# Optimization experiments

Hardware: AMD Instinct MI355X
Metric: run time of the kernel (lower is better)

## Reference

```python
import jax, jax.numpy as jnp
import numpy as np
from jax import lax

BIG = jnp.float32(1e8)  # stand-in for +inf (no zeros found yet)
EPS_W = 1e-3
SMOOTH = 1e-6
ALPHA = 0.6
BETA = 1.0


def _scan_dist(zmask):
    # zmask: (H, B, W) bool, True where pixel == 0.
    # Forward 1D chamfer pass along leading axis: exact 1D distance to nearest zero.
    def body(c, z):
        d = jnp.where(z, jnp.float32(0.0), c + jnp.float32(1.0))
        return d, d
    init = jnp.full(zmask.shape[1:], BIG, jnp.float32)
    _, out = lax.scan(body, init, zmask)
    return out  # (H, B, W)


def edt(t):
    # Exact Euclidean distance transform (distance to nearest zero), t: (B, H, W).
    # Separable Felzenszwalb-style: exact 1D pass along H, then lower-envelope
    # (brute-force min via scan) along W on squared distances.
    z = (t == 0)
    zm = jnp.moveaxis(z, 1, 0)                      # (H, B, W)
    fwd = _scan_dist(zm)
    bwd = _scan_dist(zm[::-1])[::-1]
    d1 = jnp.minimum(fwd, bwd)                      # 1D distance along H
    g = jnp.minimum(d1 * d1, BIG)                   # squared, (H, B, W)

    W = g.shape[-1]
    ys = jnp.arange(W, dtype=jnp.float32)
    g_cols = jnp.moveaxis(g, 2, 0)                  # (W, H, B)

    def body2(carry, xs):
        gcol, j = xs                                # gcol: (H, B)
        cand = gcol[..., None] + (ys - j) ** 2      # (H, B, W)
        return jnp.minimum(carry, cand), None

    init = jnp.full(g.shape, BIG, jnp.float32)
    out, _ = lax.scan(body2, init, (g_cols, ys))    # (H, B, W) squared EDT
    return jnp.sqrt(jnp.moveaxis(out, 1, 0))        # (B, H, W)


def setup_inputs() -> dict:
    key = jax.random.key(0)
    k1, k2 = jax.random.split(key)
    B, C, H, W = 16, 1, 512, 512
    inputs = jax.random.normal(k1, (B, C, H, W), dtype=jnp.float32)
    targets = jax.random.randint(k2, (B, C, H, W), 0, 2).astype(jnp.float32)
    return {"inputs": inputs, "targets": targets}


def reference(inputs, targets):
    B = targets.shape[0]
    t2d = targets[:, 0]                             # (B, H, W), squeeze channel
    w_edt = edt(t2d)                                # per-sample EDT, (B, H, W)
    v = jnp.max(w_edt, axis=(1, 2))                 # scalar max per sample
    # Faithful to original (buggy) indexing: w = v - w_edt[b] (row b, shape (W,))
    rows = w_edt[jnp.arange(B), jnp.arange(B), :]   # (B, W)
    mask = (w_edt != 0).astype(jnp.float32)         # (B, H, W)
    w = mask * (v[:, None, None] - rows[:, None, :]) + jnp.float32(EPS_W)
    weight = lax.stop_gradient(w)[:, None, :, :]    # (B, 1, H, W); no grad (numpy in orig)

    wmse = jnp.mean(weight * (inputs - targets) ** 2)

    p = jax.nn.sigmoid(inputs).reshape(-1)
    tg = targets.reshape(-1)
    intersection = jnp.sum(p * tg)
    union = jnp.sum(p) + jnp.sum(tg)
    dice = 1.0 - (2.0 * intersection + SMOOTH) / (union + SMOOTH)

    return (ALPHA * wmse, BETA * dice)
```

## Files before the change

kernel.cpp:

```cpp
#include <hip/hip_runtime.h>

#define W      512
#define IMG    (512 * 512)
#define NB     16
#define NPIX   (NB * IMG)

#define TILE_H 16
#define APRON  4
#define LROWS  (TILE_H + 2 * APRON)
#define BLOCK  1024
#define GRID   (NB * (W / TILE_H))

struct WS {
    unsigned int vmax[16];
    float C[NB * W];
    float rows[NB * W];
    float4 partial[GRID];
};
#define MEMSET_BYTES (sizeof(unsigned int) * 16 + sizeof(float) * NB * W)

__device__ __forceinline__ unsigned pk_min_u16(unsigned a, unsigned b) {
    unsigned r; asm("v_pk_min_u16 %0, %1, %2" : "=v"(r) : "v"(a), "v"(b)); return r;
}
__device__ __forceinline__ unsigned pk_max_u16(unsigned a, unsigned b) {
    unsigned r; asm("v_pk_max_u16 %0, %1, %2" : "=v"(r) : "v"(a), "v"(b)); return r;
}

__device__ int exact_best(const float* __restrict__ img, int h, int y) {
    int best = 100000000;
    for (int gh = 0; gh < W; ++gh) {
        int dhh = gh - h;
        if (dhh * dhh >= best) continue;
        const float* rp = img + (gh << 9);
        for (int yy = 0; yy < W; ++yy)
            if (rp[yy] == 0.0f) {
                int dx = yy - y;
                best = min(best, dhh * dhh + dx * dx);
            }
    }
    return best;
}

__global__ __launch_bounds__(BLOCK, 8) void fused_kernel(const float* __restrict__ inp,
                                                         const float* __restrict__ tgt,
                                                         WS* __restrict__ ws) {
    __shared__ unsigned long long zm[LROWS][10];
    __shared__ unsigned short Dd[LROWS][W];
    __shared__ float4 csh[8][128];
    __shared__ float4 ssum[BLOCK / 64];
    __shared__ unsigned smax[BLOCK / 64];

    int bid  = blockIdx.x;
    int b    = bid >> 5;
    int tile = bid & 31;
    int h0   = tile * TILE_H;
    int tid  = threadIdx.x;
    int wave = tid >> 6, lane = tid & 63;
    const float* img = tgt + (size_t)b * IMG;

    float av[4];
    #pragma unroll
    for (int j = 0; j < 4; ++j) {
        int aa = (wave << 2) + j;
        int ar = aa >> 3;
        int lr = ar < 4 ? ar : ar + 16;
        int wc = aa & 7;
        int gh = h0 - APRON + lr;
        av[j] = (gh >= 0 && gh < W) ? img[(gh << 9) + (wc << 6) + lane] : 1.0f;
    }

    size_t base4 = (size_t)b * (IMG / 4) + (size_t)tile * (TILE_H * W / 4);
    const float4* x4 = (const float4*)inp + base4;
    const float4* t4 = (const float4*)tgt + base4;

    float s0 = 0.f, s1 = 0.f, s2 = 0.f, s3 = 0.f;
    float4 ct = make_float4(0.f, 0.f, 0.f, 0.f);
    #pragma unroll
    for (int k = 0; k < 2; ++k) {
        int i = tid + (k << 10);
        float4 xv = x4[i];
        float4 tv = t4[i];
        { float d = xv.x - tv.x; float e2 = d * d; s0 += e2; ct.x += tv.x * e2;
          float p = 1.0f / (1.0f + __expf(-xv.x)); s1 += p * tv.x; s2 += p; s3 += tv.x; }
        { float d = xv.y - tv.y; float e2 = d * d; s0 += e2; ct.y += tv.y * e2;
          float p = 1.0f / (1.0f + __expf(-xv.y)); s1 += p * tv.y; s2 += p; s3 += tv.y; }
        { float d = xv.z - tv.z; float e2 = d * d; s0 += e2; ct.z += tv.z * e2;
          float p = 1.0f / (1.0f + __expf(-xv.z)); s1 += p * tv.z; s2 += p; s3 += tv.z; }
        { float d = xv.w - tv.w; float e2 = d * d; s0 += e2; ct.w += tv.w * e2;
          float p = 1.0f / (1.0f + __expf(-xv.w)); s1 += p * tv.w; s2 += p; s3 += tv.w; }

        unsigned nib = (tv.x == 0.f ? 1u : 0u) | (tv.y == 0.f ? 2u : 0u)
                     | (tv.z == 0.f ? 4u : 0u) | (tv.w == 0.f ? 8u : 0u);
        unsigned long long contrib = (unsigned long long)nib << ((lane & 15) << 2);
        #pragma unroll
        for (int m = 1; m <= 8; m <<= 1) contrib |= __shfl_xor(contrib, m);
        if ((lane & 15) == 0) {
            int r = (wave >> 1) + (k << 3);
            zm[APRON + r][((wave & 1) << 2) + (lane >> 4) + 1] = contrib;
        }
    }
    csh[tid >> 7][tid & 127] = ct;
    #pragma unroll
    for (int o = 32; o > 0; o >>= 1) {
        s0 += __shfl_down(s0, o); s1 += __shfl_down(s1, o);
        s2 += __shfl_down(s2, o); s3 += __shfl_down(s3, o);
    }
    if (lane == 0) ssum[wave] = make_float4(s0, s1, s2, s3);

    #pragma unroll
    for (int j = 0; j < 4; ++j) {
        int aa = (wave << 2) + j;
        int ar = aa >> 3;
        int lr = ar < 4 ? ar : ar + 16;
        int wc = aa & 7;
        unsigned long long m = __ballot(av[j] == 0.0f);
        if (lane == 0) zm[lr][wc + 1] = m;
    }
    if (tid < LROWS) { zm[tid][0] = 0ULL; zm[tid][9] = 0ULL; }
    __syncthreads();

    for (int u = wave; u < LROWS * 8; u += BLOCK / 64) {
        int lr = u >> 3, wc = u & 7;
        unsigned long long Wm = zm[lr][wc];
        unsigned long long Wc = zm[lr][wc + 1];
        unsigned long long Wp = zm[lr][wc + 2];
        int off = lane;
        unsigned long long wr = (Wc >> off) | (off ? (Wp << (64 - off)) : 0ULL);
        int dr = wr ? __builtin_ctzll(wr) : 1000;
        unsigned long long vl = off ? ((Wc << (64 - off)) | (Wm >> off)) : Wm;
        int dl = vl ? (1 + __builtin_clzll(vl)) : 1000;
        int d = min(min(dr, dl), 1000);
        int dd = min(d * d, 65471);
        Dd[lr][(wc << 6) + lane] = (unsigned short)dd;
    }

    if (tid < 128) {
        float4 a = csh[0][tid];
        #pragma unroll
        for (int g = 1; g < 8; ++g) {
            float4 c = csh[g][tid];
            a.x += c.x; a.y += c.y; a.z += c.z; a.w += c.w;
        }
        float* Cb = ws->C + (b << 9) + (tid << 2);
        atomicAdd(Cb + 0, a.x);
        atomicAdd(Cb + 1, a.y);
        atomicAdd(Cb + 2, a.z);
        atomicAdd(Cb + 3, a.w);
    } else if (tid == 128) {
        float4 a = ssum[0];
        #pragma unroll
        for (int i = 1; i < BLOCK / 64; ++i) {
            a.x += ssum[i].x; a.y += ssum[i].y; a.z += ssum[i].z; a.w += ssum[i].w;
        }
        ws->partial[bid] = a;
    }
    __syncthreads();

    int p = tid & 255;
    int q = tid >> 8;
    const unsigned* Dd32 = (const unsigned*)&Dd[0][0];
    const unsigned* basep = Dd32 + (q << 10) + p;
    unsigned col[12];
    #pragma unroll
    for (int j = 0; j < 12; ++j) col[j] = basep[j * 256];

    unsigned best[4];
    #pragma unroll
    for (int m = 0; m < 4; ++m) {
        unsigned bb = 0xFFFFFFFFu;
        #pragma unroll
        for (int j = 0; j <= 8; ++j) {
            unsigned dh2 = (unsigned)((j - 4) * (j - 4));
            bb = pk_min_u16(bb, col[m + j] + dh2 * 0x00010001u);
        }
        best[m] = bb;
    }
    unsigned bpk = pk_max_u16(pk_max_u16(best[0], best[1]), pk_max_u16(best[2], best[3]));
    unsigned tmax = max(bpk & 0xFFFFu, bpk >> 16);

    if (__builtin_expect(tmax > 16u, 0)) {
        tmax = 0;
        for (int m = 0; m < 4; ++m) {
            int k = (q << 2) + m;
            unsigned nb = 0;
            for (int half = 0; half < 2; ++half) {
                int y = (p << 1) + half;
                int bb = 1 << 30;
                for (int j = 0; j <= 8; ++j)
                    bb = min(bb, (j - 4) * (j - 4) + (int)Dd[k + j][y]);
                if (bb > 16) bb = exact_best(img, h0 + k, y);
                tmax = max(tmax, (unsigned)bb);
                nb |= ((unsigned)bb & 0xFFFFu) << (half * 16);
            }
            best[m] = nb;
        }
    }

    if (tile == 0 && q == (b >> 2)) {
        unsigned rb = best[b & 3];
        ws->rows[(b << 9) + (p << 1)]     = sqrtf((float)(rb & 0xFFFFu));
        ws->rows[(b << 9) + (p << 1) + 1] = sqrtf((float)(rb >> 16));
    }

    #pragma unroll
    for (int o = 32; o > 0; o >>= 1) tmax = max(tmax, (unsigned)__shfl_down(tmax, o));
    if (lane == 0) smax[wave] = tmax;
    __syncthreads();
    if (tid == 0) {
        unsigned bm = smax[0];
        #pragma unroll
        for (int i = 1; i < BLOCK / 64; ++i) bm = max(bm, smax[i]);
        atomicMax(&ws->vmax[b], bm);
    }
}

#define FBLOCK 256
__global__ __launch_bounds__(FBLOCK) void final_kernel(const WS* __restrict__ ws,
                                                       float* __restrict__ out) {
    int tid = threadIdx.x;
    __shared__ float vsh[16];
    if (tid < 16) vsh[tid] = sqrtf((float)ws->vmax[tid]);
    __syncthreads();

    double wm = 0.0;
    #pragma unroll
    for (int j = 0; j < (NB * W) / FBLOCK; ++j) {
        int cell = tid + j * FBLOCK;
        wm += (double)ws->C[cell] * (double)(vsh[cell >> 9] - ws->rows[cell]);
    }
    double e = 0, s1 = 0, s2 = 0, s3 = 0;
    #pragma unroll
    for (int j = 0; j < GRID / FBLOCK; ++j) {
        float4 p = ws->partial[tid + j * FBLOCK];
        e += p.x; s1 += p.y; s2 += p.z; s3 += p.w;
    }

    #pragma unroll
    for (int o = 32; o > 0; o >>= 1) {
        wm += __shfl_down(wm, o); e  += __shfl_down(e, o);
        s1 += __shfl_down(s1, o); s2 += __shfl_down(s2, o); s3 += __shfl_down(s3, o);
    }
    __shared__ double shd[FBLOCK / 64][5];
    int lane = tid & 63, wid = tid >> 6;
    if (lane == 0) { shd[wid][0] = wm; shd[wid][1] = e;
                     shd[wid][2] = s1; shd[wid][3] = s2; shd[wid][4] = s3; }
    __syncthreads();
    if (tid == 0) {
        double a0 = 0, a1 = 0, a2 = 0, a3 = 0, a4 = 0;
        #pragma unroll
        for (int i = 0; i < FBLOCK / 64; ++i) {
            a0 += shd[i][0]; a1 += shd[i][1]; a2 += shd[i][2]; a3 += shd[i][3]; a4 += shd[i][4];
        }
        double wmse = (a0 + 0.001 * a1) / (double)NPIX;
        out[0] = (float)(0.6 * wmse);
        out[1] = (float)(1.0 - (2.0 * a2 + 1e-6) / (a3 + a4 + 1e-6));
    }
}

extern "C" void kernel_launch(void* const* d_in, const int* in_sizes, int n_in,
                              void* d_out, int out_size, void* d_ws, size_t ws_size,
                              hipStream_t stream) {
    const float* inp = (const float*)d_in[0];
    const float* tgt = (const float*)d_in[1];
    float* out = (float*)d_out;
    WS* ws = (WS*)d_ws;

    hipMemsetAsync(d_ws, 0, MEMSET_BYTES, stream);
    fused_kernel<<<GRID, BLOCK, 0, stream>>>(inp, tgt, ws);
    final_kernel<<<1, FBLOCK, 0, stream>>>(ws, out);
}
```

Baseline: 90.10 us.

## Replace atomics and memset with per-block partials and multi-block final reduction

Each fused block now writes its column partial sums, per-wave scalar sums and per-wave maxima to dedicated workspace slots instead of using float atomicAdd/atomicMax. This removes the hipMemsetAsync launch and the in-block reduction syncs. The final kernel runs one block per image to reduce those partials, and the last block, found through a wrap-around atomic counter, combines the 16 per-image results. This trades atomic contention and a memset for more workspace traffic and a counter that is never reset, which relies on the modulo-16 check staying valid across calls.

New measurement: 90.76 us. No clear change (+0.7%).

```diff
diff --git a/kernel.cpp b/kernel.cpp
--- a/kernel.cpp
+++ b/kernel.cpp
@@ -12,12 +12,13 @@
 #define GRID   (NB * (W / TILE_H))
 
 struct WS {
-    unsigned int vmax[16];
-    float C[NB * W];
     float rows[NB * W];
-    float4 partial[GRID];
+    float4 colpart[GRID][128];
+    float4 partial[GRID][16];
+    unsigned wsmax[GRID][16];
+    double img5[NB][5];
+    unsigned counter;
 };
-#define MEMSET_BYTES (sizeof(unsigned int) * 16 + sizeof(float) * NB * W)
 
 __device__ __forceinline__ unsigned pk_min_u16(unsigned a, unsigned b) {
     unsigned r; asm("v_pk_min_u16 %0, %1, %2" : "=v"(r) : "v"(a), "v"(b)); return r;
@@ -47,8 +48,6 @@
     __shared__ unsigned long long zm[LROWS][10];
     __shared__ unsigned short Dd[LROWS][W];
     __shared__ float4 csh[8][128];
-    __shared__ float4 ssum[BLOCK / 64];
-    __shared__ unsigned smax[BLOCK / 64];
 
     int bid  = blockIdx.x;
     int b    = bid >> 5;
@@ -105,7 +104,7 @@
         s0 += __shfl_down(s0, o); s1 += __shfl_down(s1, o);
         s2 += __shfl_down(s2, o); s3 += __shfl_down(s3, o);
     }
-    if (lane == 0) ssum[wave] = make_float4(s0, s1, s2, s3);
+    if (lane == 0) ws->partial[bid][wave] = make_float4(s0, s1, s2, s3);
 
     #pragma unroll
     for (int j = 0; j < 4; ++j) {
@@ -141,18 +140,7 @@
             float4 c = csh[g][tid];
             a.x += c.x; a.y += c.y; a.z += c.z; a.w += c.w;
         }
-        float* Cb = ws->C + (b << 9) + (tid << 2);
-        atomicAdd(Cb + 0, a.x);
-        atomicAdd(Cb + 1, a.y);
-        atomicAdd(Cb + 2, a.z);
-        atomicAdd(Cb + 3, a.w);
-    } else if (tid == 128) {
-        float4 a = ssum[0];
-        #pragma unroll
-        for (int i = 1; i < BLOCK / 64; ++i) {
-            a.x += ssum[i].x; a.y += ssum[i].y; a.z += ssum[i].z; a.w += ssum[i].w;
-        }
-        ws->partial[bid] = a;
+        ws->colpart[bid][tid] = a;
     }
     __syncthreads();
 
@@ -204,52 +192,83 @@
 
     #pragma unroll
     for (int o = 32; o > 0; o >>= 1) tmax = max(tmax, (unsigned)__shfl_down(tmax, o));
-    if (lane == 0) smax[wave] = tmax;
-    __syncthreads();
-    if (tid == 0) {
-        unsigned bm = smax[0];
-        #pragma unroll
-        for (int i = 1; i < BLOCK / 64; ++i) bm = max(bm, smax[i]);
-        atomicMax(&ws->vmax[b], bm);
-    }
+    if (lane == 0) ws->wsmax[bid][wave] = tmax;
 }
 
 #define FBLOCK 256
-__global__ __launch_bounds__(FBLOCK) void final_kernel(const WS* __restrict__ ws,
+__global__ __launch_bounds__(FBLOCK) void final_kernel(WS* __restrict__ ws,
                                                        float* __restrict__ out) {
-    int tid = threadIdx.x;
-    __shared__ float vsh[16];
-    if (tid < 16) vsh[tid] = sqrtf((float)ws->vmax[tid]);
-    __syncthreads();
-
-    double wm = 0.0;
-    #pragma unroll
-    for (int j = 0; j < (NB * W) / FBLOCK; ++j) {
-        int cell = tid + j * FBLOCK;
-        wm += (double)ws->C[cell] * (double)(vsh[cell >> 9] - ws->rows[cell]);
-    }
-    double e = 0, s1 = 0, s2 = 0, s3 = 0;
-    #pragma unroll
-    for (int j = 0; j < GRID / FBLOCK; ++j) {
-        float4 p = ws->partial[tid + j * FBLOCK];
-        e += p.x; s1 += p.y; s2 += p.z; s3 += p.w;
-    }
+    int b    = blockIdx.x;
+    int tid  = threadIdx.x;
+    int lane = tid & 63, wave = tid >> 6;
+    __shared__ unsigned vsh4[4];
+    __shared__ double shd[4][5];
+    __shared__ double fin[80];
+    __shared__ int sh_last;
+
+    unsigned vm = 0;
+    #pragma unroll
+    for (int j = 0; j < 2; ++j) {
+        int idx = (tid << 1) + j;
+        vm = max(vm, ws->wsmax[(b << 5) + (idx >> 4)][idx & 15]);
+    }
+    #pragma unroll
+    for (int o = 32; o > 0; o >>= 1) vm = max(vm, (unsigned)__shfl_down(vm, o));
+    if (lane == 0) vsh4[wave] = vm;
+    __syncthreads();
+    float v = sqrtf((float)max(max(vsh4[0], vsh4[1]), max(vsh4[2], vsh4[3])));
+
+    double e = 0, t1 = 0, t2 = 0, t3 = 0;
+    #pragma unroll
+    for (int j = 0; j < 2; ++j) {
+        int idx = (tid << 1) + j;
+        float4 pp = ws->partial[(b << 5) + (idx >> 4)][idx & 15];
+        e += pp.x; t1 += pp.y; t2 += pp.z; t3 += pp.w;
+    }
+
+    int y4 = tid & 127, half = tid >> 7;
+    float4 acc = make_float4(0.f, 0.f, 0.f, 0.f);
+    #pragma unroll
+    for (int t = 0; t < 16; ++t) {
+        float4 cp = ws->colpart[(b << 5) + (half << 4) + t][y4];
+        acc.x += cp.x; acc.y += cp.y; acc.z += cp.z; acc.w += cp.w;
+    }
+    const float4 r4 = *(const float4*)&ws->rows[(b << 9) + (y4 << 2)];
+    double wm = (double)acc.x * (double)(v - r4.x) + (double)acc.y * (double)(v - r4.y)
+              + (double)acc.z * (double)(v - r4.z) + (double)acc.w * (double)(v - r4.w);
 
     #pragma unroll
     for (int o = 32; o > 0; o >>= 1) {
         wm += __shfl_down(wm, o); e  += __shfl_down(e, o);
-        s1 += __shfl_down(s1, o); s2 += __shfl_down(s2, o); s3 += __shfl_down(s3, o);
-    }
-    __shared__ double shd[FBLOCK / 64][5];
-    int lane = tid & 63, wid = tid >> 6;
-    if (lane == 0) { shd[wid][0] = wm; shd[wid][1] = e;
-                     shd[wid][2] = s1; shd[wid][3] = s2; shd[wid][4] = s3; }
+        t1 += __shfl_down(t1, o); t2 += __shfl_down(t2, o); t3 += __shfl_down(t3, o);
+    }
+    if (lane == 0) { shd[wave][0] = wm; shd[wave][1] = e;
+                     shd[wave][2] = t1; shd[wave][3] = t2; shd[wave][4] = t3; }
     __syncthreads();
     if (tid == 0) {
         double a0 = 0, a1 = 0, a2 = 0, a3 = 0, a4 = 0;
         #pragma unroll
-        for (int i = 0; i < FBLOCK / 64; ++i) {
+        for (int i = 0; i < 4; ++i) {
             a0 += shd[i][0]; a1 += shd[i][1]; a2 += shd[i][2]; a3 += shd[i][3]; a4 += shd[i][4];
+        }
+        ws->img5[b][0] = a0; ws->img5[b][1] = a1; ws->img5[b][2] = a2;
+        ws->img5[b][3] = a3; ws->img5[b][4] = a4;
+        __threadfence();
+        unsigned old = atomicAdd(&ws->counter, 1u);
+        sh_last = (((old + 1) & 15) == 0);
+    }
+    __syncthreads();
+    if (!sh_last) return;
+
+    __threadfence();
+    if (tid < 80) fin[tid] = ((volatile double*)ws->img5)[tid];
+    __syncthreads();
+    if (tid == 0) {
+        double a0 = 0, a1 = 0, a2 = 0, a3 = 0, a4 = 0;
+        #pragma unroll
+        for (int i = 0; i < 16; ++i) {
+            a0 += fin[i * 5 + 0]; a1 += fin[i * 5 + 1]; a2 += fin[i * 5 + 2];
+            a3 += fin[i * 5 + 3]; a4 += fin[i * 5 + 4];
         }
         double wmse = (a0 + 0.001 * a1) / (double)NPIX;
         out[0] = (float)(0.6 * wmse);
@@ -265,7 +284,6 @@
     float* out = (float*)d_out;
     WS* ws = (WS*)d_ws;
 
-    hipMemsetAsync(d_ws, 0, MEMSET_BYTES, stream);
     fused_kernel<<<GRID, BLOCK, 0, stream>>>(inp, tgt, ws);
-    final_kernel<<<1, FBLOCK, 0, stream>>>(ws, out);
-}
+    final_kernel<<<NB, FBLOCK, 0, stream>>>(ws, out);
+}
```
